# Optimization experiments

Measured on AMD Instinct MI355X. Metric: run time of the kernel, lower is better.

The kernel has to match this reference:

```python
import jax, jax.numpy as jnp
import numpy as np

B, T, C = 4, 2048, 1024
H = 16
D = C // H          # 64 head dim
CS = 128            # chunk_size (hard-coded in module)


def setup_inputs() -> dict:
    key = jax.random.key(0)
    ks = jax.random.split(key, 6)
    scale = 0.02
    x = jax.random.normal(ks[0], (B, T, C), dtype=jnp.float32)
    Wq = jax.random.normal(ks[1], (C, C), dtype=jnp.float32) * scale
    Wk = jax.random.normal(ks[2], (C, C), dtype=jnp.float32) * scale
    Wv = jax.random.normal(ks[3], (C, C), dtype=jnp.float32) * scale
    Wo = jax.random.normal(ks[4], (C, C), dtype=jnp.float32) * scale
    alpha_raw = jnp.zeros((1, H, 1, 1), dtype=jnp.float32)
    beta_raw = jnp.zeros((1, H, 1, 1), dtype=jnp.float32)
    return {"x": x, "Wq": Wq, "Wk": Wk, "Wv": Wv, "Wo": Wo,
            "alpha_raw": alpha_raw, "beta_raw": beta_raw}


def reference(x, Wq, Wk, Wv, Wo, alpha_raw, beta_raw):
    Bb, Tt, Cc = x.shape
    nc = Tt // CS
    N = Bb * H * nc  # flattened (batch, head, chunk) recurrence lanes

    # projections -> [B, H, T, D]
    def proj(W):
        return (x @ W).reshape(Bb, Tt, H, D).transpose(0, 2, 1, 3)
    q, k, v = proj(Wq), proj(Wk), proj(Wv)
    # F.normalize(k, dim=-1) with eps=1e-12
    k = k / jnp.maximum(jnp.linalg.norm(k, axis=-1, keepdims=True), 1e-12)

    alpha = jax.nn.sigmoid(alpha_raw).reshape(H) * 0.5  # [H]
    beta = jax.nn.sigmoid(beta_raw).reshape(H) * 0.5    # [H]
    a = jnp.broadcast_to(alpha[None, :, None], (Bb, H, nc)).reshape(N, 1, 1)
    b = jnp.broadcast_to(beta[None, :, None], (Bb, H, nc)).reshape(N, 1, 1)

    # chunk layout [CS, N, D] for time-major scan
    def to_scan(u):
        return u.reshape(Bb, H, nc, CS, D).reshape(N, CS, D).transpose(1, 0, 2)
    qc, kc, vc = to_scan(q), to_scan(k), to_scan(v)

    # --- per-chunk operators: A = prod(I - a k k^T), B accumulates writes ---
    def op_step(carry, kv):
        A, Bo = carry
        kt, vt = kv  # [N, D]
        Ak = jnp.einsum('nij,nj->ni', A, kt)
        A = A - a * (Ak[:, :, None] * kt[:, None, :])
        Bk = jnp.einsum('nij,nj->ni', Bo, kt)
        Bo = Bo - a * (Bk[:, :, None] * kt[:, None, :]) + b * (vt[:, :, None] * kt[:, None, :])
        return (A, Bo), None

    A0 = jnp.broadcast_to(jnp.eye(D, dtype=x.dtype), (N, D, D))
    (Aop, Bop), _ = jax.lax.scan(op_step, (A0, jnp.zeros((N, D, D), x.dtype)), (kc, vc))

    # --- inter-chunk scan: M_{i+1} = M_i A_i + B_i ---
    Aop_c = Aop.reshape(Bb, H, nc, D, D).transpose(2, 0, 1, 3, 4)
    Bop_c = Bop.reshape(Bb, H, nc, D, D).transpose(2, 0, 1, 3, 4)

    def chunk_step(M, ab):
        Ai, Bi = ab
        return jnp.einsum('bhij,bhjk->bhik', M, Ai) + Bi, M

    M_final, M_starts = jax.lax.scan(
        chunk_step, jnp.zeros((Bb, H, D, D), x.dtype), (Aop_c, Bop_c))

    # --- intra-chunk application: y_t = M_t q_t; rank-1 delta update ---
    M0 = M_starts.transpose(1, 2, 0, 3, 4).reshape(N, D, D)

    def proc_step(M, qkv):
        qt, kt, vt = qkv
        yt = jnp.einsum('nij,nj->ni', M, qt)  # == q_t @ M^T (inference path)
        Mk = jnp.einsum('nij,nj->ni', M, kt)
        M = M - a * (Mk[:, :, None] * kt[:, None, :]) + b * (vt[:, :, None] * kt[:, None, :])
        return M, yt

    _, ys = jax.lax.scan(proc_step, M0, (qc, kc, vc))  # [CS, N, D]
    y = ys.transpose(1, 0, 2).reshape(Bb, H, Tt, D)
    y = y.transpose(0, 2, 1, 3).reshape(Bb, Tt, Cc)
    y = y @ Wo  # c_proj (dropout=0 -> identity)
    return (y, M_final)
```

## Files before the change

kernel.cpp:

```cpp
#include <hip/hip_runtime.h>
#include <stdint.h>


#define DEV __device__ __forceinline__

typedef __attribute__((ext_vector_type(4))) float f32x4;
typedef __attribute__((ext_vector_type(8))) __bf16 bf16x8;
typedef __attribute__((ext_vector_type(4))) __bf16 bf16x4;

typedef const __attribute__((address_space(1))) uint32_t* gas1_t;
typedef __attribute__((address_space(3))) uint32_t* las3_t;

DEV void gload_lds16(const void* g, void* l) {
  __builtin_amdgcn_global_load_lds((gas1_t)g, (las3_t)l, 16, 0, 0);
}

DEV float sgm(float x) { return 1.f / (1.f + __expf(-x)); }

template <int CTRL>
DEV float dpp_mov(float x) {
  return __builtin_bit_cast(
      float, __builtin_amdgcn_mov_dpp(__builtin_bit_cast(int, x), CTRL, 0xF, 0xF, true));
}
DEV float row16_reduce(float x) {
  x += dpp_mov<0x121>(x);
  x += dpp_mov<0x122>(x);
  x += dpp_mov<0x124>(x);
  x += dpp_mov<0x128>(x);
  return x;
}

DEV int swzb(int row, int col, int stride) {
  return ((row * stride + col) << 1) ^ ((row & 7) << 4);
}
DEV bf16x8 ldfrag(const __bf16* B, int row, int col, int stride) {
  return *(const bf16x8*)((const char*)B + swzb(row, col, stride));
}
DEV __bf16 ldsc(const __bf16* B, int row, int col, int stride) {
  return *(const __bf16*)((const char*)B + swzb(row, col, stride));
}
DEV void stb(__bf16* B, int row, int col, int stride, __bf16 v) {
  *(__bf16*)((char*)B + swzb(row, col, stride)) = v;
}
DEV void stb4(__bf16* B, int row, int c4, int stride, bf16x4 v) {
  *(bf16x4*)((char*)B + swzb(row, c4, stride)) = v;
}
DEV int goffn(int tr) {
  int m = tr >> 1;
  return (tr & 1) ? (2 * m * m + 4 * m + 2) : (2 * m * m + 2 * m);
}
DEV int stile(int tr, int sc) { return ((tr * (tr + 1)) / 2 + sc) * 256; }

__global__ __launch_bounds__(256) void cast_f32_bf16(const float* __restrict__ in,
                                                     __bf16* __restrict__ out) {
  int idx = blockIdx.x * 256 + threadIdx.x;
  float4 v = ((const float4*)in)[idx];
  bf16x4 o;
  o[0] = (__bf16)v.x; o[1] = (__bf16)v.y; o[2] = (__bf16)v.z; o[3] = (__bf16)v.w;
  ((bf16x4*)out)[idx] = o;
}

__global__ __launch_bounds__(256) void transpose_cast(const float* __restrict__ W,
                                                      __bf16* __restrict__ Wt) {
  __shared__ float tile[32][33];
  int tx = threadIdx.x & 31, ty = threadIdx.x >> 5;
  int n0 = blockIdx.x * 32, k0 = blockIdx.y * 32;
#pragma unroll
  for (int u = 0; u < 4; ++u)
    tile[ty + u * 8][tx] = W[(size_t)(k0 + ty + u * 8) * 1024 + n0 + tx];
  __syncthreads();
#pragma unroll
  for (int u = 0; u < 4; ++u)
    Wt[(size_t)(n0 + ty + u * 8) * 1024 + k0 + tx] = (__bf16)tile[tx][ty + u * 8];
}

__global__ __launch_bounds__(256) void gemm_bt(const __bf16* __restrict__ A,
                                               const __bf16* __restrict__ Bt,
                                               float* __restrict__ Cf,
                                               __bf16* __restrict__ Cb, int mode) {
  const int t = threadIdx.x;
  const int wv = t >> 6, lane = t & 63;
  const int bm = blockIdx.y, bn = blockIdx.x;
  const int K = 1024;
  __shared__ __bf16 lA[4096];
  __shared__ __bf16 lB[4096];
  f32x4 acc[4][4];
#pragma unroll
  for (int m = 0; m < 4; ++m)
#pragma unroll
    for (int n = 0; n < 4; ++n) acc[m][n] = 0.f;
  const int wr = wv >> 1, wc = wv & 1;
  const int fr = lane & 15, fk = (lane >> 4) * 8;
  const int e0 = (wv * 128 + lane) * 8;
  const int e1 = (wv * 128 + 64 + lane) * 8;
  const int r0s = e0 >> 5, c0s = e0 & 31;
  const int r1s = e1 >> 5, c1s = e1 & 31;
  for (int k0 = 0; k0 < K; k0 += 32) {
    gload_lds16(A + (size_t)(bm * 128 + r0s) * K + k0 + c0s, lA + wv * 1024);
    gload_lds16(Bt + (size_t)(bn * 128 + r0s) * K + k0 + c0s, lB + wv * 1024);
    gload_lds16(A + (size_t)(bm * 128 + r1s) * K + k0 + c1s, lA + wv * 1024 + 512);
    gload_lds16(Bt + (size_t)(bn * 128 + r1s) * K + k0 + c1s, lB + wv * 1024 + 512);
    __syncthreads();
    bf16x8 af[4], bg[4];
#pragma unroll
    for (int m = 0; m < 4; ++m)
      af[m] = *(const bf16x8*)(lA + (wr * 64 + m * 16 + fr) * 32 + fk);
#pragma unroll
    for (int n = 0; n < 4; ++n)
      bg[n] = *(const bf16x8*)(lB + (wc * 64 + n * 16 + fr) * 32 + fk);
#pragma unroll
    for (int m = 0; m < 4; ++m)
#pragma unroll
      for (int n = 0; n < 4; ++n)
        acc[m][n] = __builtin_amdgcn_mfma_f32_16x16x32_bf16(af[m], bg[n], acc[m][n], 0, 0, 0);
    __syncthreads();
  }
  const int rr = (lane >> 4) * 4, cl = lane & 15;
#pragma unroll
  for (int m = 0; m < 4; ++m) {
#pragma unroll
    for (int n = 0; n < 4; ++n) {
#pragma unroll
      for (int rg = 0; rg < 4; ++rg) {
        int row = bm * 128 + wr * 64 + m * 16 + rr + rg;
        int col = bn * 128 + wc * 64 + n * 16 + cl;
        float val = acc[m][n][rg];
        if (mode == 0) {
          Cf[(size_t)row * 1024 + col] = val;
        } else {
          int buf = col >> 10, cc = col & 1023;
          int b = row >> 11, tk = row & 2047;
          int h = cc >> 6, d = cc & 63;
          Cb[(size_t)buf * 8388608 + (((size_t)b * 16 + h) * 2048 + tk) * 64 + d] =
              (__bf16)val;
        }
      }
    }
  }
}

__global__ __launch_bounds__(512, 6) void wy_ab(const __bf16* __restrict__ kb,
                                                const __bf16* __restrict__ vb,
                                                const float* __restrict__ ar,
                                                const float* __restrict__ br,
                                                __bf16* __restrict__ Ug,
                                                __bf16* __restrict__ Wgb,
                                                __bf16* __restrict__ ATg,
                                                __bf16* __restrict__ Bop) {
  int n = blockIdx.x, h = (n >> 4) & 15;
  float a = sgm(ar[h]) * 0.5f;
  float b = sgm(br[h]) * 0.5f;
  int t = threadIdx.x, wid = t >> 6, lane = t & 63;
  int fr = lane & 15, fkq = lane >> 4, fk = fkq * 8;
  __shared__ __attribute__((aligned(16))) char pool[51200];
  __bf16* Ks  = (__bf16*)pool;
  __bf16* MTu = (__bf16*)pool;
  __bf16* MTw = (__bf16*)(pool + 16384);
  __bf16* Sng = (__bf16*)(pool + 32768);
  __bf16* KT  = (__bf16*)(pool + 32768);
  const __bf16* kg = kb + (size_t)n * 8192;
  const __bf16* vg = vb + (size_t)n * 8192;
  bf16x8 zz;
#pragma unroll
  for (int e = 0; e < 8; ++e) zz[e] = (__bf16)0.f;
  f32x4 c0 = {0.f, 0.f, 0.f, 0.f};
  bf16x4 kreg[4];
#pragma unroll
  for (int it = 0; it < 4; ++it) {
    int u = it * 512 + t;
    int row = u >> 4, c4 = (u & 15) * 4;
    bf16x4 kh = ((const bf16x4*)kg)[u];
    float kf[4];
#pragma unroll
    for (int e = 0; e < 4; ++e) kf[e] = (float)kh[e];
    float ssq = kf[0] * kf[0] + kf[1] * kf[1] + kf[2] * kf[2] + kf[3] * kf[3];
    ssq = row16_reduce(ssq);
    float inv = 1.f / fmaxf(sqrtf(ssq), 1e-12f);
    bf16x4 kn;
#pragma unroll
    for (int e = 0; e < 4; ++e) kn[e] = (__bf16)(kf[e] * inv);
    kreg[it] = kn;
    stb4(Ks, row, c4, 64, kn);
  }
  __syncthreads();
  for (int p = wid; p < 36; p += 8) {
    int tr = 0, pp = p;
    while (pp > tr) { pp -= (tr + 1); ++tr; }
    int sc = pp;
    f32x4 acc = {0.f, 0.f, 0.f, 0.f};
#pragma unroll
    for (int ks = 0; ks < 2; ++ks)
      acc = __builtin_amdgcn_mfma_f32_16x16x32_bf16(
          ldfrag(Ks, tr * 16 + fr, ks * 32 + fk, 64),
          ldfrag(Ks, sc * 16 + fr, ks * 32 + fk, 64), acc, 0, 0, 0);
    __bf16* dst = Sng + stile(tr, sc);
#pragma unroll
    for (int rg = 0; rg < 4; ++rg) {
      int r = fkq * 4 + rg;
      float v = -a * acc[rg];
      if (tr == sc && fr >= r) v = 0.f;
      dst[r * 16 + fr] = (__bf16)v;
    }
  }
  f32x4 U[4], W[4];
#pragma unroll
  for (int ct = 0; ct < 4; ++ct) {
#pragma unroll
    for (int rg = 0; rg < 4; ++rg) {
      int row = wid * 16 + fkq * 4 + rg, col = ct * 16 + fr;
      U[ct][rg] = (float)ldsc(Ks, row, col, 64);
      W[ct][rg] = b * (float)vg[row * 64 + col];
    }
  }
  __syncthreads();
  {
    __bf16* scr  = ((__bf16*)pool) + wid * 2048;
    __bf16* tNT  = scr;
    __bf16* tN2R = scr + 256;
    __bf16* tN2T = scr + 512;
    __bf16* tN4R = scr + 768;
    __bf16* tN4T = scr + 1024;
    __bf16* tN8T = scr + 1280;
    __bf16* tPR  = scr + 1536;
    __bf16* Nd = Sng + stile(wid, wid);
    float nv[4];
#pragma unroll
    for (int rg = 0; rg < 4; ++rg) {
      nv[rg] = (float)Nd[(fkq * 4 + rg) * 16 + fr];
      tNT[fr * 16 + fkq * 4 + rg] = (__bf16)nv[rg];
    }
    asm volatile("s_waitcnt lgkmcnt(0)" ::: "memory");
    bf16x8 af = (fk < 16) ? *(const bf16x8*)(Nd + fr * 16 + fk) : zz;
    bf16x8 bop = (fk < 16) ? *(const bf16x8*)(tNT + fr * 16 + fk) : zz;
    f32x4 X = __builtin_amdgcn_mfma_f32_16x16x32_bf16(af, bop, c0, 0, 0, 0);
#pragma unroll
    for (int rg = 0; rg < 4; ++rg) {
      __bf16 v = (__bf16)X[rg];
      tN2R[(fkq * 4 + rg) * 16 + fr] = v;
      tN2T[fr * 16 + fkq * 4 + rg] = v;
    }
    asm volatile("s_waitcnt lgkmcnt(0)" ::: "memory");
    af = (fk < 16) ? *(const bf16x8*)(tN2R + fr * 16 + fk) : zz;
    bop = (fk < 16) ? *(const bf16x8*)(tN2T + fr * 16 + fk) : zz;
    X = __builtin_amdgcn_mfma_f32_16x16x32_bf16(af, bop, c0, 0, 0, 0);
#pragma unroll
    for (int rg = 0; rg < 4; ++rg) {
      __bf16 v = (__bf16)X[rg];
      tN4R[(fkq * 4 + rg) * 16 + fr] = v;
      tN4T[fr * 16 + fkq * 4 + rg] = v;
    }
    asm volatile("s_waitcnt lgkmcnt(0)" ::: "memory");
    af = (fk < 16) ? *(const bf16x8*)(tN4R + fr * 16 + fk) : zz;
    bop = (fk < 16) ? *(const bf16x8*)(tN4T + fr * 16 + fk) : zz;
    X = __builtin_amdgcn_mfma_f32_16x16x32_bf16(af, bop, c0, 0, 0, 0);
#pragma unroll
    for (int rg = 0; rg < 4; ++rg)
      tN8T[fr * 16 + fkq * 4 + rg] = (__bf16)X[rg];
    f32x4 P;
#pragma unroll
    for (int rg = 0; rg < 4; ++rg)
      P[rg] = ((fkq * 4 + rg) == fr ? 1.f : 0.f) + nv[rg];
#pragma unroll
    for (int d = 0; d < 3; ++d) {
      const __bf16* tB = (d == 0) ? tN2T : (d == 1) ? tN4T : tN8T;
#pragma unroll
      for (int rg = 0; rg < 4; ++rg)
        tPR[(fkq * 4 + rg) * 16 + fr] = (__bf16)P[rg];
      asm volatile("s_waitcnt lgkmcnt(0)" ::: "memory");
      af = (fk < 16) ? *(const bf16x8*)(tPR + fr * 16 + fk) : zz;
      bop = (fk < 16) ? *(const bf16x8*)(tB + fr * 16 + fk) : zz;
      P = __builtin_amdgcn_mfma_f32_16x16x32_bf16(af, bop, P, 0, 0, 0);
    }
#pragma unroll
    for (int rg = 0; rg < 4; ++rg)
      Nd[(fkq * 4 + rg) * 16 + fr] = (__bf16)P[rg];
  }
  __syncthreads();
  for (int bb = 0; bb < 8; ++bb) {
    if (wid == bb) {
#pragma unroll
      for (int ct = 0; ct < 4; ++ct) {
        bf16x4 uu, ww;
#pragma unroll
        for (int rg = 0; rg < 4; ++rg) {
          uu[rg] = (__bf16)U[ct][rg];
          ww[rg] = (__bf16)W[ct][rg];
        }
        stb4(MTu, ct * 16 + fr, bb * 16 + fkq * 4, 128, uu);
        stb4(MTw, ct * 16 + fr, bb * 16 + fkq * 4, 128, ww);
      }
      asm volatile("s_waitcnt lgkmcnt(0)" ::: "memory");
      const __bf16* invT = Sng + stile(bb, bb);
      bf16x8 afv = (fk < 16) ? *(const bf16x8*)(invT + fr * 16 + fk) : zz;
#pragma unroll
      for (int ct = 0; ct < 4; ++ct) {
        bf16x8 bu = (fk < 16) ? ldfrag(MTu, ct * 16 + fr, bb * 16 + fk, 128) : zz;
        bf16x8 bw = (fk < 16) ? ldfrag(MTw, ct * 16 + fr, bb * 16 + fk, 128) : zz;
        U[ct] = __builtin_amdgcn_mfma_f32_16x16x32_bf16(afv, bu, c0, 0, 0, 0);
        W[ct] = __builtin_amdgcn_mfma_f32_16x16x32_bf16(afv, bw, c0, 0, 0, 0);
      }
#pragma unroll
      for (int ct = 0; ct < 4; ++ct) {
        bf16x4 uu, ww;
#pragma unroll
        for (int rg = 0; rg < 4; ++rg) {
          uu[rg] = (__bf16)U[ct][rg];
          ww[rg] = (__bf16)W[ct][rg];
        }
        stb4(MTu, ct * 16 + fr, bb * 16 + fkq * 4, 128, uu);
        stb4(MTw, ct * 16 + fr, bb * 16 + fkq * 4, 128, ww);
      }
    }
    __syncthreads();
    if (wid > bb) {
      bf16x8 af = zz;
      if (fk < 16) af = *(const bf16x8*)(Sng + stile(wid, bb) + fr * 16 + fk);
#pragma unroll
      for (int ct = 0; ct < 4; ++ct) {
        bf16x8 bu = zz, bw = zz;
        if (fk < 16) {
          bu = ldfrag(MTu, ct * 16 + fr, bb * 16 + fk, 128);
          bw = ldfrag(MTw, ct * 16 + fr, bb * 16 + fk, 128);
        }
        U[ct] = __builtin_amdgcn_mfma_f32_16x16x32_bf16(af, bu, U[ct], 0, 0, 0);
        W[ct] = __builtin_amdgcn_mfma_f32_16x16x32_bf16(af, bw, W[ct], 0, 0, 0);
      }
    }
  }
#pragma unroll
  for (int it = 0; it < 4; ++it) {
    int u = it * 512 + t;
    int row = u >> 4, c4 = (u & 15) * 4;
#pragma unroll
    for (int e = 0; e < 4; ++e) stb(KT, c4 + e, row, 128, kreg[it][e]);
  }
  __bf16* ugo = Ug + (size_t)n * 8192;
  __bf16* wgo = Wgb + (size_t)n * 8192;
#pragma unroll
  for (int ct = 0; ct < 4; ++ct)
#pragma unroll
    for (int rg = 0; rg < 4; ++rg) {
      int row = wid * 16 + fkq * 4 + rg, col = ct * 16 + fr;
      ugo[row * 64 + col] = (__bf16)U[ct][rg];
      wgo[row * 64 + col] = (__bf16)W[ct][rg];
    }
  __syncthreads();
#pragma unroll
  for (int q = 0; q < 4; ++q) {
    int tile = wid + q * 8;
    int mat = tile >> 4;
    int ti = (tile >> 2) & 3, tj = tile & 3;
    f32x4 acc = {0.f, 0.f, 0.f, 0.f};
    if (mat == 0) {
#pragma unroll
      for (int ks = 0; ks < 4; ++ks)
        acc = __builtin_amdgcn_mfma_f32_16x16x32_bf16(
            ldfrag(KT, ti * 16 + fr, ks * 32 + fk, 128),
            ldfrag(MTu, tj * 16 + fr, ks * 32 + fk, 128), acc, 0, 0, 0);
      char* dst = (char*)(ATg + (size_t)n * 4096);
#pragma unroll
      for (int rg = 0; rg < 4; ++rg) {
        int i = ti * 16 + fkq * 4 + rg, j = tj * 16 + fr;
        float v = (i == j ? 1.f : 0.f) - a * acc[rg];
        *(__bf16*)(dst + swzb(i, j, 64)) = (__bf16)v;
      }
    } else {
#pragma unroll
      for (int ks = 0; ks < 4; ++ks)
        acc = __builtin_amdgcn_mfma_f32_16x16x32_bf16(
            ldfrag(MTw, ti * 16 + fr, ks * 32 + fk, 128),
            ldfrag(KT, tj * 16 + fr, ks * 32 + fk, 128), acc, 0, 0, 0);
      __bf16* dst = Bop + (size_t)n * 4096;
#pragma unroll
      for (int rg = 0; rg < 4; ++rg)
        dst[(ti * 16 + fkq * 4 + rg) * 64 + tj * 16 + fr] = (__bf16)acc[rg];
    }
  }
}

__global__ __launch_bounds__(512) void chunk_scan(const __bf16* __restrict__ ATg,
                                                  const __bf16* __restrict__ Bop,
                                                  __bf16* __restrict__ Mst,
                                                  float* __restrict__ Mfinal) {
  int bh = blockIdx.x;
  int t = threadIdx.x, wid = t >> 6, lane = t & 63;
  int fr = lane & 15, fkq = lane >> 4, fk = fkq * 8;
  int ti = wid & 3, tj0 = (wid >> 2) << 1;
  __shared__ __bf16 Mh[4096];
  __shared__ __bf16 Ml[4096];
  __shared__ __bf16 At[2][4096];
  f32x4 acc[2];
  acc[0] = 0.f;
  acc[1] = 0.f;
  gload_lds16(ATg + (size_t)bh * 16 * 4096 + t * 8, At[0] + t * 8);
  for (int c = 0; c < 16; ++c) {
    int cur = c & 1;
    if (c < 15)
      gload_lds16(ATg + ((size_t)(bh * 16 + c + 1)) * 4096 + t * 8,
                  At[cur ^ 1] + t * 8);
    __bf16* mstc = Mst + ((size_t)(bh * 16 + c)) * 4096;
#pragma unroll
    for (int p = 0; p < 2; ++p) {
      int tj = tj0 + p;
#pragma unroll
      for (int rg = 0; rg < 4; ++rg) {
        int row = ti * 16 + fkq * 4 + rg, col = tj * 16 + fr;
        float v = acc[p][rg];
        __bf16 hi = (__bf16)v;
        mstc[row * 64 + col] = hi;
        stb(Mh, row, col, 64, hi);
        stb(Ml, row, col, 64, (__bf16)(v - (float)hi));
      }
    }
    __syncthreads();
    size_t bb = ((size_t)(bh * 16 + c)) * 4096;
#pragma unroll
    for (int p = 0; p < 2; ++p) {
      int tj = tj0 + p;
      f32x4 na;
#pragma unroll
      for (int rg = 0; rg < 4; ++rg)
        na[rg] = (float)Bop[bb + (ti * 16 + fkq * 4 + rg) * 64 + tj * 16 + fr];
#pragma unroll
      for (int ks = 0; ks < 2; ++ks) {
        bf16x8 bfrag = ldfrag(At[cur], tj * 16 + fr, ks * 32 + fk, 64);
        bf16x8 ah = ldfrag(Mh, ti * 16 + fr, ks * 32 + fk, 64);
        bf16x8 al = ldfrag(Ml, ti * 16 + fr, ks * 32 + fk, 64);
        na = __builtin_amdgcn_mfma_f32_16x16x32_bf16(ah, bfrag, na, 0, 0, 0);
        na = __builtin_amdgcn_mfma_f32_16x16x32_bf16(al, bfrag, na, 0, 0, 0);
      }
      acc[p] = na;
    }
    __syncthreads();
  }
#pragma unroll
  for (int p = 0; p < 2; ++p) {
    int tj = tj0 + p;
#pragma unroll
    for (int rg = 0; rg < 4; ++rg)
      Mfinal[(size_t)bh * 4096 + (ti * 16 + fkq * 4 + rg) * 64 + tj * 16 + fr] =
          acc[p][rg];
  }
}

__global__ __launch_bounds__(512, 4) void y_assemble(const __bf16* __restrict__ qb,
                                                     const __bf16* __restrict__ kb,
                                                     const __bf16* __restrict__ Ug,
                                                     const __bf16* __restrict__ Wgb,
                                                     const __bf16* __restrict__ Mst,
                                                     const float* __restrict__ ar,
                                                     __bf16* __restrict__ ybf) {
  int n = blockIdx.x, h = (n >> 4) & 15, b = n >> 8, c = n & 15;
  float a = sgm(ar[h]) * 0.5f;
  int t = threadIdx.x, wid = t >> 6, lane = t & 63;
  int fr = lane & 15, fk = (lane >> 4) * 8;
  __shared__ __bf16 Qs[8192];
  __shared__ __bf16 Rs[8192];
  __shared__ __bf16 M0s[4096];
  __shared__ __bf16 Gs[10240];
  __shared__ __bf16 WtT[8192];
  const __bf16* qg = qb + (size_t)n * 8192;
  const __bf16* kg = kb + (size_t)n * 8192;
  const __bf16* mg = Mst + (size_t)n * 4096;
#pragma unroll
  for (int it = 0; it < 4; ++it) {
    int u = it * 512 + t;
    int row = u >> 4, c4 = (u & 15) * 4;
    stb4(Qs, row, c4, 64, ((const bf16x4*)qg)[u]);
    bf16x4 kh = ((const bf16x4*)kg)[u];
    float kf[4];
#pragma unroll
    for (int e = 0; e < 4; ++e) kf[e] = (float)kh[e];
    float ssq = kf[0] * kf[0] + kf[1] * kf[1] + kf[2] * kf[2] + kf[3] * kf[3];
    ssq = row16_reduce(ssq);
    float inv = 1.f / fmaxf(sqrtf(ssq), 1e-12f);
    bf16x4 kn;
#pragma unroll
    for (int e = 0; e < 4; ++e) kn[e] = (__bf16)(kf[e] * inv);
    stb4(Rs, row, c4, 64, kn);
  }
#pragma unroll
  for (int it = 0; it < 2; ++it) {
    int u = it * 512 + t;
    int row = u >> 4, c4 = (u & 15) * 4;
    stb4(M0s, row, c4, 64, ((const bf16x4*)mg)[u]);
  }
#pragma unroll
  for (int pz = 0; pz < 2; ++pz) {
    int e = pz * 512 + t;
    int m = e >> 8, idx = e & 255;
    Gs[(2 * m * m + 4 * m + 1) * 256 + idx] = (__bf16)0.f;
  }
  __syncthreads();
  for (int p = wid; p < 36; p += 8) {
    int tr = 0, pp = p;
    while (pp > tr) { pp -= (tr + 1); ++tr; }
    int sc = pp;
    f32x4 acc = {0.f, 0.f, 0.f, 0.f};
#pragma unroll
    for (int ks = 0; ks < 2; ++ks)
      acc = __builtin_amdgcn_mfma_f32_16x16x32_bf16(
          ldfrag(Qs, tr * 16 + fr, ks * 32 + fk, 64),
          ldfrag(Rs, sc * 16 + fr, ks * 32 + fk, 64), acc, 0, 0, 0);
    int row0 = (lane >> 4) * 4, col = lane & 15;
    __bf16* gt = Gs + (goffn(tr) + sc) * 256;
#pragma unroll
    for (int rg = 0; rg < 4; ++rg) {
      int r = row0 + rg;
      float v = acc[rg];
      if (tr == sc && col >= r) v = 0.f;
      gt[r * 16 + col] = (__bf16)v;
    }
  }
  __syncthreads();
  const __bf16* ug = Ug + (size_t)n * 8192;
  const __bf16* wg = Wgb + (size_t)n * 8192;
#pragma unroll
  for (int it = 0; it < 4; ++it) {
    int u = it * 512 + t;
    int row = u >> 4, c4 = (u & 15) * 4;
    stb4(Rs, row, c4, 64, ((const bf16x4*)ug)[u]);
  }
  __syncthreads();
#pragma unroll
  for (int q = 0; q < 4; ++q) {
    int tile = wid + q * 8;
    int ti = tile >> 2, tj = tile & 3;
    f32x4 acc = {0.f, 0.f, 0.f, 0.f};
#pragma unroll
    for (int ks = 0; ks < 2; ++ks)
      acc = __builtin_amdgcn_mfma_f32_16x16x32_bf16(
          ldfrag(Rs, ti * 16 + fr, ks * 32 + fk, 64),
          ldfrag(M0s, tj * 16 + fr, ks * 32 + fk, 64), acc, 0, 0, 0);
    int row0 = (lane >> 4) * 4, col = lane & 15;
#pragma unroll
    for (int rg = 0; rg < 4; ++rg) {
      int s = ti * 16 + row0 + rg, i = tj * 16 + col;
      float wv = (float)wg[s * 64 + i];
      stb(WtT, i, s, 128, (__bf16)(wv - a * acc[rg]));
    }
  }
  __syncthreads();
  __bf16* yg = ybf + ((size_t)(b * 2048 + c * 128)) * 1024 + h * 64;
#pragma unroll
  for (int q = 0; q < 4; ++q) {
    int tile = wid + q * 8;
    int ti = tile >> 2, tj = tile & 3;
    f32x4 acc = {0.f, 0.f, 0.f, 0.f};
#pragma unroll
    for (int ks = 0; ks < 2; ++ks)
      acc = __builtin_amdgcn_mfma_f32_16x16x32_bf16(
          ldfrag(Qs, ti * 16 + fr, ks * 32 + fk, 64),
          ldfrag(M0s, tj * 16 + fr, ks * 32 + fk, 64), acc, 0, 0, 0);
    int goffv = goffn(ti);
    int np = (ti + 2) >> 1;
    for (int ks = 0; ks < np; ++ks) {
      int gtile = goffv + ks * 2 + (fk >> 4);
      bf16x8 af = *(const bf16x8*)(Gs + gtile * 256 + fr * 16 + (fk & 15));
      acc = __builtin_amdgcn_mfma_f32_16x16x32_bf16(
          af, ldfrag(WtT, tj * 16 + fr, ks * 32 + fk, 128), acc, 0, 0, 0);
    }
    int row0 = (lane >> 4) * 4, col = lane & 15;
#pragma unroll
    for (int rg = 0; rg < 4; ++rg) {
      int tt = ti * 16 + row0 + rg, d = tj * 16 + col;
      yg[(size_t)tt * 1024 + d] = (__bf16)acc[rg];
    }
  }
}

extern "C" void kernel_launch(void* const* d_in, const int* in_sizes, int n_in,
                              void* d_out, int out_size, void* d_ws, size_t ws_size,
                              hipStream_t stream) {
  const float* x  = (const float*)d_in[0];
  const float* Wq = (const float*)d_in[1];
  const float* Wk = (const float*)d_in[2];
  const float* Wv = (const float*)d_in[3];
  const float* Wo = (const float*)d_in[4];
  const float* ar = (const float*)d_in[5];
  const float* br = (const float*)d_in[6];

  char* ws = (char*)d_ws;
  __bf16* xb    = (__bf16*)ws;
  __bf16* ybf   = xb;
  __bf16* wqkvt = (__bf16*)(ws + (17u << 20));
  __bf16* wot   = (__bf16*)(ws + (23u << 20));
  __bf16* qb    = (__bf16*)(ws + (25u << 20));
  __bf16* kb    = qb + 8388608;
  __bf16* vb    = kb + 8388608;
  __bf16* Ugb   = (__bf16*)(ws + (76u << 20));
  __bf16* Wgb   = (__bf16*)(ws + (93u << 20));
  __bf16* ATg   = (__bf16*)(ws + (110u << 20));
  __bf16* Bop   = (__bf16*)(ws + (127u << 20));
  __bf16* Mst   = (__bf16*)(ws + (144u << 20));

  float* yout = (float*)d_out;
  float* Mfin = yout + 8388608;

  cast_f32_bf16<<<8192, 256, 0, stream>>>(x, xb);
  dim3 tg(32, 32);
  transpose_cast<<<tg, 256, 0, stream>>>(Wq, wqkvt);
  transpose_cast<<<tg, 256, 0, stream>>>(Wk, wqkvt + (1u << 20));
  transpose_cast<<<tg, 256, 0, stream>>>(Wv, wqkvt + (2u << 20));
  transpose_cast<<<tg, 256, 0, stream>>>(Wo, wot);

  dim3 gqkv(24, 64);
  gemm_bt<<<gqkv, 256, 0, stream>>>(xb, wqkvt, nullptr, qb, 1);

  wy_ab<<<1024, 512, 0, stream>>>(kb, vb, ar, br, Ugb, Wgb, ATg, Bop);
  chunk_scan<<<64, 512, 0, stream>>>(ATg, Bop, Mst, Mfin);
  y_assemble<<<1024, 512, 0, stream>>>(qb, kb, Ugb, Wgb, Mst, ar, ybf);

  dim3 go(8, 64);
  gemm_bt<<<go, 256, 0, stream>>>(ybf, wot, yout, nullptr, 0);
}
```

Before: 212.9 us.

## Rewrite bf16 GEMM with 256x128 tiles, double-buffered LDS, swizzle and XCD remap

Measured after the change: 212.6 us. Within noise of the previous version (-0.1%).

```diff
diff --git a/kernel.cpp b/kernel.cpp
--- a/kernel.cpp
+++ b/kernel.cpp
@@ -74,57 +74,77 @@
     Wt[(size_t)(n0 + ty + u * 8) * 1024 + k0 + tx] = (__bf16)tile[tx][ty + u * 8];
 }
 
-__global__ __launch_bounds__(256) void gemm_bt(const __bf16* __restrict__ A,
-                                               const __bf16* __restrict__ Bt,
-                                               float* __restrict__ Cf,
-                                               __bf16* __restrict__ Cb, int mode) {
+template <int CALLS>
+DEV void stage_tile(const __bf16* __restrict__ G, __bf16* L, int t, int wid, int K) {
+#pragma unroll
+  for (int it = 0; it < CALLS; ++it) {
+    int e = it * 512 + t;
+    int row = e >> 3;
+    int c0 = ((e & 7) ^ (row & 7)) << 3;
+    gload_lds16(G + (size_t)row * K + c0, L + it * 4096 + wid * 512);
+  }
+}
+
+__global__ __launch_bounds__(512, 2) void gemm_bt(const __bf16* __restrict__ A,
+                                                  const __bf16* __restrict__ Bt,
+                                                  float* __restrict__ Cf,
+                                                  __bf16* __restrict__ Cb,
+                                                  int mode, int NBN) {
   const int t = threadIdx.x;
-  const int wv = t >> 6, lane = t & 63;
-  const int bm = blockIdx.y, bn = blockIdx.x;
+  const int wid = t >> 6, lane = t & 63;
+  const int fr = lane & 15, fkq = lane >> 4, fk = fkq * 8;
+  const int wr = wid >> 2, wc = wid & 3;
   const int K = 1024;
-  __shared__ __bf16 lA[4096];
-  __shared__ __bf16 lB[4096];
-  f32x4 acc[4][4];
-#pragma unroll
-  for (int m = 0; m < 4; ++m)
-#pragma unroll
-    for (int n = 0; n < 4; ++n) acc[m][n] = 0.f;
-  const int wr = wv >> 1, wc = wv & 1;
-  const int fr = lane & 15, fk = (lane >> 4) * 8;
-  const int e0 = (wv * 128 + lane) * 8;
-  const int e1 = (wv * 128 + 64 + lane) * 8;
-  const int r0s = e0 >> 5, c0s = e0 & 31;
-  const int r1s = e1 >> 5, c1s = e1 & 31;
-  for (int k0 = 0; k0 < K; k0 += 32) {
-    gload_lds16(A + (size_t)(bm * 128 + r0s) * K + k0 + c0s, lA + wv * 1024);
-    gload_lds16(Bt + (size_t)(bn * 128 + r0s) * K + k0 + c0s, lB + wv * 1024);
-    gload_lds16(A + (size_t)(bm * 128 + r1s) * K + k0 + c1s, lA + wv * 1024 + 512);
-    gload_lds16(Bt + (size_t)(bn * 128 + r1s) * K + k0 + c1s, lB + wv * 1024 + 512);
+  int nwg = gridDim.x, lin = blockIdx.x;
+  int q = nwg >> 3;
+  int id2 = (lin & 7) * q + (lin >> 3);
+  int bn = id2 % NBN, bm = id2 / NBN;
+  __shared__ __bf16 lA[2][16384];
+  __shared__ __bf16 lB[2][8192];
+  const __bf16* Ab = A + (size_t)(bm * 256) * K;
+  const __bf16* Bb = Bt + (size_t)(bn * 128) * K;
+  f32x4 acc[8][2];
+#pragma unroll
+  for (int m = 0; m < 8; ++m) {
+    acc[m][0] = 0.f;
+    acc[m][1] = 0.f;
+  }
+  stage_tile<4>(Ab, lA[0], t, wid, K);
+  stage_tile<2>(Bb, lB[0], t, wid, K);
+  __syncthreads();
+  for (int kt = 0; kt < 16; ++kt) {
+    int cur = kt & 1;
+    if (kt < 15) {
+      stage_tile<4>(Ab + (kt + 1) * 64, lA[cur ^ 1], t, wid, K);
+      stage_tile<2>(Bb + (kt + 1) * 64, lB[cur ^ 1], t, wid, K);
+    }
+#pragma unroll
+    for (int kk = 0; kk < 2; ++kk) {
+      bf16x8 af[8], bg[2];
+#pragma unroll
+      for (int m = 0; m < 8; ++m)
+        af[m] = ldfrag(lA[cur], wr * 128 + m * 16 + fr, kk * 32 + fk, 64);
+#pragma unroll
+      for (int nn = 0; nn < 2; ++nn)
+        bg[nn] = ldfrag(lB[cur], wc * 32 + nn * 16 + fr, kk * 32 + fk, 64);
+#pragma unroll
+      for (int m = 0; m < 8; ++m)
+#pragma unroll
+        for (int nn = 0; nn < 2; ++nn)
+          acc[m][nn] =
+              __builtin_amdgcn_mfma_f32_16x16x32_bf16(af[m], bg[nn], acc[m][nn], 0, 0, 0);
+    }
     __syncthreads();
-    bf16x8 af[4], bg[4];
-#pragma unroll
-    for (int m = 0; m < 4; ++m)
-      af[m] = *(const bf16x8*)(lA + (wr * 64 + m * 16 + fr) * 32 + fk);
-#pragma unroll
-    for (int n = 0; n < 4; ++n)
-      bg[n] = *(const bf16x8*)(lB + (wc * 64 + n * 16 + fr) * 32 + fk);
-#pragma unroll
-    for (int m = 0; m < 4; ++m)
-#pragma unroll
-      for (int n = 0; n < 4; ++n)
-        acc[m][n] = __builtin_amdgcn_mfma_f32_16x16x32_bf16(af[m], bg[n], acc[m][n], 0, 0, 0);
-    __syncthreads();
-  }
-  const int rr = (lane >> 4) * 4, cl = lane & 15;
-#pragma unroll
-  for (int m = 0; m < 4; ++m) {
-#pragma unroll
-    for (int n = 0; n < 4; ++n) {
+  }
+#pragma unroll
+  for (int m = 0; m < 8; ++m) {
+#pragma unroll
+    for (int nn = 0; nn < 2; ++nn) {
 #pragma unroll
       for (int rg = 0; rg < 4; ++rg) {
-        int row = bm * 128 + wr * 64 + m * 16 + rr + rg;
-        int col = bn * 128 + wc * 64 + n * 16 + cl;
-        float val = acc[m][n][rg];
+        int row = bm * 256 + wr * 128 + m * 16 + fkq * 4 + rg;
+        int col = bn * 128 + wc * 32 + nn * 16 + fr;
+        float val = acc[m][nn][rg];
         if (mode == 0) {
           Cf[(size_t)row * 1024 + col] = val;
         } else {
@@ -604,13 +624,11 @@
   transpose_cast<<<tg, 256, 0, stream>>>(Wv, wqkvt + (2u << 20));
   transpose_cast<<<tg, 256, 0, stream>>>(Wo, wot);
 
-  dim3 gqkv(24, 64);
-  gemm_bt<<<gqkv, 256, 0, stream>>>(xb, wqkvt, nullptr, qb, 1);
+  gemm_bt<<<768, 512, 0, stream>>>(xb, wqkvt, nullptr, qb, 1, 24);
 
   wy_ab<<<1024, 512, 0, stream>>>(kb, vb, ar, br, Ugb, Wgb, ATg, Bop);
   chunk_scan<<<64, 512, 0, stream>>>(ATg, Bop, Mst, Mfin);
   y_assemble<<<1024, 512, 0, stream>>>(qb, kb, Ugb, Wgb, Mst, ar, ybf);
 
-  dim3 go(8, 64);
-  gemm_bt<<<go, 256, 0, stream>>>(ybf, wot, yout, nullptr, 0);
-}
+  gemm_bt<<<256, 512, 0, stream>>>(ybf, wot, yout, nullptr, 0, 8);
+}
```
